# Kernel tuning notes

Measured on AMD Instinct MI355X. Metric: run time of the kernel, lower is better.

## Reference

```python
import jax, jax.numpy as jnp
import numpy as np

NUM_HEADS = 16
DIM_K = 128
DIM_V = 128
ROPE_BASE = 10000.0


def rope(x):
    # x: [..., seq, d]; rotate-half convention
    d = x.shape[-1]
    seq = x.shape[-2]
    half = d // 2
    inv_freq = 1.0 / (ROPE_BASE ** (jnp.arange(0, half, dtype=jnp.float32) / half))
    ang = jnp.arange(seq, dtype=jnp.float32)[:, None] * inv_freq[None, :]  # [seq, half]
    cos, sin = jnp.cos(ang), jnp.sin(ang)
    x1, x2 = x[..., :half], x[..., half:]
    return jnp.concatenate([x1 * cos - x2 * sin, x1 * sin + x2 * cos], axis=-1)


def setup_inputs() -> dict:
    key = jax.random.key(0)
    ks = jax.random.split(key, 8)
    B, S, D = 2, 2048, 2048
    s = lambda fan_in: 1.0 / np.sqrt(fan_in)
    return {
        'q_in': jax.random.normal(ks[0], (B, S, D), jnp.float32),
        'k_in': jax.random.normal(ks[1], (B, S, D), jnp.float32),
        'v_in': jax.random.normal(ks[2], (B, S, D), jnp.float32),
        'mask': jnp.zeros((B, S), dtype=bool),
        'Wq': jax.random.normal(ks[3], (D, NUM_HEADS * DIM_K), jnp.float32) * s(D),
        'bq': jnp.zeros((NUM_HEADS * DIM_K,), jnp.float32),
        'Wk': jax.random.normal(ks[4], (D, DIM_K), jnp.float32) * s(D),
        'bk': jnp.zeros((DIM_K,), jnp.float32),
        'Wv': jax.random.normal(ks[5], (D, DIM_V), jnp.float32) * s(D),
        'bv': jnp.zeros((DIM_V,), jnp.float32),
        'Wo': jax.random.normal(ks[6], (NUM_HEADS * DIM_V, D), jnp.float32) * s(NUM_HEADS * DIM_V),
        'bo': jnp.zeros((D,), jnp.float32),
    }


def reference(q_in, k_in, v_in, mask, Wq, bq, Wk, bk, Wv, bv, Wo, bo):
    B, Sq, _ = q_in.shape
    Sk = k_in.shape[1]
    # projections: multi-head Q, single shared K/V head (MQA)
    q = (q_in @ Wq + bq).reshape(B, Sq, NUM_HEADS, DIM_K).transpose(0, 2, 1, 3)  # [B,H,Sq,dk]
    k = k_in @ Wk + bk  # [B,Sk,dk]
    v = v_in @ Wv + bv  # [B,Sk,dv]
    # inline RoPE on q and k
    q = rope(q)
    k = rope(k)
    scores = jnp.einsum('bhqd,bkd->bhqk', q, k) / np.sqrt(DIM_K)  # [B,H,Sq,Sk]
    # padding mask: True means masked out
    scores = jnp.where(mask[:, None, None, :], -jnp.inf, scores)
    # causal mask
    causal = jnp.triu(jnp.ones((Sq, Sk), dtype=bool), k=1)
    scores = jnp.where(causal[None, None], -jnp.inf, scores)
    weights = jax.nn.softmax(scores, axis=-1)
    attn = jnp.einsum('bhqk,bkd->bhqd', weights, v)  # [B,H,Sq,dv]
    attn = attn.transpose(0, 2, 1, 3).reshape(B, Sq, NUM_HEADS * DIM_V)
    return attn @ Wo + bo
```

## Files before the change

kernel.cpp:

```cpp
#include <hip/hip_runtime.h>

#define NHEADS 16
#define DKV 128
#define BB 2
#define SS 2048
#define DD 2048

typedef __attribute__((ext_vector_type(8))) short bf16x8;
typedef __attribute__((ext_vector_type(4))) short bf16x4;
typedef __attribute__((ext_vector_type(4))) float f32x4;

#define QSCL 0.12752775f

__device__ __forceinline__ short f2bf(float x) {
  unsigned u = __builtin_bit_cast(unsigned, x);
  unsigned r = (u + 0x7fffu + ((u >> 16) & 1u)) >> 16;
  return (short)(unsigned short)r;
}
__device__ __forceinline__ float bf2f(short s) {
  unsigned u = ((unsigned)(unsigned short)s) << 16;
  return __builtin_bit_cast(float, u);
}
__device__ __forceinline__ unsigned pk2bf(float a, float b) {
#if __has_builtin(__builtin_amdgcn_cvt_pk_bf16_f32)
  typedef __attribute__((ext_vector_type(2))) __bf16 bf2_t;
  bf2_t r = __builtin_amdgcn_cvt_pk_bf16_f32(a, b);
  return __builtin_bit_cast(unsigned, r);
#else
  unsigned ua = __builtin_bit_cast(unsigned, a);
  unsigned ub = __builtin_bit_cast(unsigned, b);
  return ((ua + 0x8000u) >> 16) | ((ub + 0x8000u) & 0xffff0000u);
#endif
}
__device__ __forceinline__ float exp2fast(float x) {
#if __has_builtin(__builtin_amdgcn_exp2f)
  return __builtin_amdgcn_exp2f(x);
#else
  return exp2f(x);
#endif
}

__device__ __forceinline__ void async16(const void* g, void* l) {
  __builtin_amdgcn_global_load_lds(
      (__attribute__((address_space(1))) void*)g,
      (__attribute__((address_space(3))) void*)l, 16, 0, 0);
}

__global__ __launch_bounds__(256) void cvt_q(const float* __restrict__ x,
                                             short* __restrict__ y) {
  int idx = blockIdx.x * 256 + threadIdx.x;
  int g = idx * 8;
  float4 a = *(const float4*)(x + g);
  float4 b = *(const float4*)(x + g + 4);
  uint4 o = {pk2bf(a.x, a.y), pk2bf(a.z, a.w), pk2bf(b.x, b.y), pk2bf(b.z, b.w)};
  *(uint4*)(y + g) = o;
}

__global__ __launch_bounds__(256) void transpose_w(
    const float* __restrict__ W, short* __restrict__ Wt, int K, int N,
    float scale) {
  __shared__ float T[32][33];
  const int nt = blockIdx.x * 32;
  const int kt = blockIdx.y * 32;
  const int tx = threadIdx.x & 31;
  const int ty = threadIdx.x >> 5;
#pragma unroll
  for (int i = 0; i < 4; ++i)
    T[ty + i * 8][tx] = W[(size_t)(kt + ty + i * 8) * N + nt + tx];
  __syncthreads();
#pragma unroll
  for (int i = 0; i < 4; ++i)
    Wt[(size_t)(nt + ty + i * 8) * K + kt + tx] = f2bf(T[tx][ty + i * 8] * scale);
}

__global__ void mask_bias(const unsigned char* __restrict__ m,
                          float* __restrict__ mb) {
  int i = blockIdx.x * 256 + threadIdx.x;
  mb[i] = m[i] ? -1e30f : 0.0f;
}

template <int AMODE>
__global__ __launch_bounds__(256) void gemm_as(
    const void* __restrict__ Ap, const short* __restrict__ Bt,
    const float* __restrict__ bias, void* __restrict__ Cp,
    int M, int N, int K, int KC, int cmode, float bscale) {
  __shared__ __align__(16) short As[128 * 32];
  __shared__ __align__(16) short Bs[128 * 32];
  const int tid = threadIdx.x;
  const int bm = blockIdx.y * 128;
  const int bn = blockIdx.x * 128;
  const int kz = blockIdx.z;
  const int w = tid >> 6, lane = tid & 63;
  const int lm = lane & 15, q4 = lane >> 4;
  const int m0 = (w & 1) * 64, n0 = (w >> 1) * 64;

  f32x4 acc[4][4];
#pragma unroll
  for (int mi = 0; mi < 4; ++mi)
#pragma unroll
    for (int ni = 0; ni < 4; ++ni) acc[mi][ni] = (f32x4){0.f, 0.f, 0.f, 0.f};

  const int kbeg = kz * KC;
  const int kend = kbeg + KC;

  for (int k0 = kbeg; k0 < kend; k0 += 32) {
    __syncthreads();
    if (AMODE == 1) {
      const short* Ab = (const short*)Ap;
#pragma unroll
      for (int i = 0; i < 2; ++i) {
        int rA = (w * 2 + i) * 16 + (lane >> 2);
        int cA = (lane & 3) ^ (rA & 3);
        async16(Ab + (size_t)(bm + rA) * K + k0 + cA * 8, &As[(w * 2 + i) * 512]);
      }
    } else {
      const float* Af = (const float*)Ap;
      float4 av[4];
#pragma unroll
      for (int i = 0; i < 4; ++i) {
        int qd = tid + i * 256;
        int r = qd >> 3, cq = qd & 7;
        av[i] = *(const float4*)(Af + (size_t)(bm + r) * K + k0 + cq * 4);
      }
#pragma unroll
      for (int i = 0; i < 4; ++i) {
        int qd = tid + i * 256;
        int r = qd >> 3, cq = qd & 7;
        int ch = cq >> 1, hf = cq & 1;
        int pc = ch ^ (r & 3);
        bf16x4 t = {f2bf(av[i].x), f2bf(av[i].y), f2bf(av[i].z), f2bf(av[i].w)};
        *(bf16x4*)&As[r * 32 + pc * 8 + hf * 4] = t;
      }
    }
#pragma unroll
    for (int i = 0; i < 2; ++i) {
      int rB = (w * 2 + i) * 16 + (lane >> 2);
      int cB = (lane & 3) ^ (rB & 3);
      async16(Bt + (size_t)(bn + rB) * K + k0 + cB * 8, &Bs[(w * 2 + i) * 512]);
    }
    __syncthreads();

    bf16x8 af[4], bf[4];
#pragma unroll
    for (int mi = 0; mi < 4; ++mi)
      af[mi] = *(const bf16x8*)&As[(m0 + mi * 16 + lm) * 32 + ((q4 ^ (lm & 3)) * 8)];
#pragma unroll
    for (int ni = 0; ni < 4; ++ni)
      bf[ni] = *(const bf16x8*)&Bs[(n0 + ni * 16 + lm) * 32 + ((q4 ^ (lm & 3)) * 8)];
#pragma unroll
    for (int mi = 0; mi < 4; ++mi)
#pragma unroll
      for (int ni = 0; ni < 4; ++ni)
        acc[mi][ni] = __builtin_amdgcn_mfma_f32_16x16x32_bf16(
            af[mi], bf[ni], acc[mi][ni], 0, 0, 0);
  }

  if (cmode == 2) {
    float* Cf = (float*)Cp + (size_t)kz * M * N;
#pragma unroll
    for (int mi = 0; mi < 4; ++mi)
#pragma unroll
      for (int ni = 0; ni < 4; ++ni)
#pragma unroll
        for (int reg = 0; reg < 4; ++reg)
          Cf[(size_t)(bm + m0 + mi * 16 + q4 * 4 + reg) * N +
             (bn + n0 + ni * 16 + lm)] = acc[mi][ni][reg];
  } else {
#pragma unroll
    for (int mi = 0; mi < 4; ++mi)
#pragma unroll
      for (int ni = 0; ni < 4; ++ni)
#pragma unroll
        for (int reg = 0; reg < 4; ++reg) {
          int rowg = bm + m0 + mi * 16 + q4 * 4 + reg;
          int colg = bn + n0 + ni * 16 + lm;
          float val = acc[mi][ni][reg] + bias[colg] * bscale;
          if (cmode == 0)
            ((float*)Cp)[(size_t)rowg * N + colg] = val;
          else
            ((short*)Cp)[(size_t)rowg * N + colg] = f2bf(val);
        }
  }
}

#define SPLITK 4
__global__ __launch_bounds__(256) void kv_reduce(
    const float* __restrict__ kpart, const float* __restrict__ vpart,
    const float* __restrict__ bk, const float* __restrict__ bv,
    short* __restrict__ kp, short* __restrict__ vtb) {
  __shared__ float Kt[32][128];
  __shared__ short Vl[128][36];
  const int tid = threadIdx.x;
  const int r0 = blockIdx.x * 32;
#pragma unroll
  for (int i = 0; i < 16; ++i) {
    int e = tid + i * 256;
    int r = e >> 7, c = e & 127;
    float sk = 0.f, sv = 0.f;
#pragma unroll
    for (int z = 0; z < SPLITK; ++z) {
      sk += kpart[((size_t)z * 4096 + r0 + r) * 128 + c];
      sv += vpart[((size_t)z * 4096 + r0 + r) * 128 + c];
    }
    Kt[r][c] = sk + bk[c];
    Vl[c][r] = f2bf(sv + bv[c]);
  }
  __syncthreads();
#pragma unroll
  for (int i = 0; i < 8; ++i) {
    int e = tid + i * 256;
    int r = e >> 6, d = e & 63;
    float x1 = Kt[r][d], x2 = Kt[r][d + 64];
    float s = (float)((r0 + r) & (SS - 1));
    float ang = s * exp2fast((float)d * (-13.287712379549449f / 64.0f));
    float sn, cs;
    __sincosf(ang, &sn, &cs);
    kp[(size_t)(r0 + r) * 128 + d] = f2bf(x1 * cs - x2 * sn);
    kp[(size_t)(r0 + r) * 128 + d + 64] = f2bf(x1 * sn + x2 * cs);
  }
  const int b = r0 >> 11;
  const int j = tid >> 1, soff = (tid & 1) * 16;
  short* dst = vtb + ((size_t)b * 128 + j) * SS + (r0 & (SS - 1)) + soff;
#pragma unroll
  for (int t = 0; t < 2; ++t) {
    bf16x8 tmp;
#pragma unroll
    for (int u = 0; u < 8; ++u) tmp[u] = Vl[j][soff + t * 8 + u];
    *(bf16x8*)(dst + t * 8) = tmp;
  }
}

__global__ __launch_bounds__(256) void rope_q(short* __restrict__ qp) {
  int idx = blockIdx.x * 256 + threadIdx.x;
  int j8 = idx & 7;
  int h = (idx >> 3) & (NHEADS - 1);
  int s = (idx >> 7) & (SS - 1);
  int b = idx >> 18;
  short* base = qp + (((size_t)b * SS + s) * NHEADS + h) * DKV + j8 * 8;
  bf16x8 x1 = *(bf16x8*)base;
  bf16x8 x2 = *(bf16x8*)(base + 64);
  bf16x8 y1, y2;
#pragma unroll
  for (int j = 0; j < 8; ++j) {
    int d = j8 * 8 + j;
    float ang = (float)s * exp2fast((float)d * (-13.287712379549449f / 64.0f));
    float sn, cs;
    __sincosf(ang, &sn, &cs);
    float a = bf2f(x1[j]), bb2 = bf2f(x2[j]);
    y1[j] = f2bf(a * cs - bb2 * sn);
    y2[j] = f2bf(a * sn + bb2 * cs);
  }
  *(bf16x8*)base = y1;
  *(bf16x8*)(base + 64) = y2;
}

#define PSTR 40

__global__ __launch_bounds__(256, 2) void flash_kernel(
    const short* __restrict__ q, const short* __restrict__ k,
    const short* __restrict__ vt, const float* __restrict__ mb,
    short* __restrict__ out) {
  __shared__ __align__(16) short Kb[2][32 * 128];
  __shared__ __align__(16) short Vb[2][128 * 64];
  __shared__ __align__(16) short Ps[4][32 * PSTR];
  const int h = blockIdx.y, b = blockIdx.z;
  const int qx = b ? (int)blockIdx.x : 15 - (int)blockIdx.x;
  const int tid = threadIdx.x;
  const int w = tid >> 6, lane = tid & 63;
  const int lm = lane & 15, q4 = lane >> 4;
  const int qrow0 = qx * 128 + w * 32;

  bf16x8 qf[2][4];
#pragma unroll
  for (int ni = 0; ni < 2; ++ni)
#pragma unroll
    for (int ks = 0; ks < 4; ++ks)
      qf[ni][ks] = *(const bf16x8*)(q +
          ((size_t)b * SS + qrow0 + ni * 16 + lm) * (NHEADS * DKV) + h * DKV +
          ks * 32 + q4 * 8);

  bf16x8 onesb;
#pragma unroll
  for (int j = 0; j < 8; ++j) onesb[j] = (short)0x3F80;

  f32x4 O[8][2], Ol[2];
#pragma unroll
  for (int vi = 0; vi < 8; ++vi)
#pragma unroll
    for (int ni = 0; ni < 2; ++ni) O[vi][ni] = (f32x4){0.f, 0.f, 0.f, 0.f};
#pragma unroll
  for (int ni = 0; ni < 2; ++ni) Ol[ni] = (f32x4){0.f, 0.f, 0.f, 0.f};

  const int ktmax = 4 * qx + 4;
  const size_t kbase = (size_t)b * SS;

  {
#pragma unroll
    for (int i = 0; i < 2; ++i) {
      int r = (w * 2 + i) * 4 + (lane >> 4);
      int c = (lane & 15) ^ (r & 7);
      async16(k + (kbase + r) * DKV + c * 8, &Kb[0][(w * 2 + i) * 512]);
    }
#pragma unroll
    for (int i = 0; i < 4; ++i) {
      int rV = (w * 4 + i) * 8 + (lane >> 3);
      int cV = (lane & 7) ^ (rV & 7);
      async16(vt + ((size_t)b * DKV + rV) * SS + cV * 8, &Vb[0][(w * 4 + i) * 512]);
    }
  }
  f32x4 mc0 = *(const f32x4*)(mb + kbase + q4 * 4);
  f32x4 mc1 = *(const f32x4*)(mb + kbase + 16 + q4 * 4);

  for (int kt = 0; kt < ktmax; ++kt) {
    __syncthreads();

    f32x4 mn0, mn1;
    if (kt + 1 < ktmax) {
      const int t = kt + 1;
#pragma unroll
      for (int i = 0; i < 2; ++i) {
        int r = (w * 2 + i) * 4 + (lane >> 4);
        int c = (lane & 15) ^ (r & 7);
        async16(k + (kbase + (size_t)t * 32 + r) * DKV + c * 8,
                &Kb[t & 1][(w * 2 + i) * 512]);
      }
      if (kt & 1) {
#pragma unroll
        for (int i = 0; i < 4; ++i) {
          int rV = (w * 4 + i) * 8 + (lane >> 3);
          int cV = (lane & 7) ^ (rV & 7);
          async16(vt + ((size_t)b * DKV + rV) * SS + (size_t)t * 32 + cV * 8,
                  &Vb[(t >> 1) & 1][(w * 4 + i) * 512]);
        }
      }
      mn0 = *(const f32x4*)(mb + kbase + (size_t)t * 32 + q4 * 4);
      mn1 = *(const f32x4*)(mb + kbase + (size_t)t * 32 + 16 + q4 * 4);
    }

    const short* Kc = Kb[kt & 1];
    f32x4 sacc[2][2];
#pragma unroll
    for (int mi = 0; mi < 2; ++mi)
#pragma unroll
      for (int ni = 0; ni < 2; ++ni) sacc[mi][ni] = (f32x4){0.f, 0.f, 0.f, 0.f};
#pragma unroll
    for (int mi = 0; mi < 2; ++mi)
#pragma unroll
      for (int ks = 0; ks < 4; ++ks) {
        bf16x8 kf = *(const bf16x8*)&Kc[(mi * 16 + lm) * 128 +
                                        (((ks * 4 + q4) ^ (lm & 7)) << 3)];
#pragma unroll
        for (int ni = 0; ni < 2; ++ni)
          sacc[mi][ni] = __builtin_amdgcn_mfma_f32_16x16x32_bf16(
              kf, qf[ni][ks], sacc[mi][ni], 0, 0, 0);
      }

    const bool diag = (kt >= 4 * qx);
#pragma unroll
    for (int mi = 0; mi < 2; ++mi) {
      f32x4 mbv = mi ? mc1 : mc0;
#pragma unroll
      for (int ni = 0; ni < 2; ++ni) {
        float pv[4];
#pragma unroll
        for (int reg = 0; reg < 4; ++reg) {
          float s = sacc[mi][ni][reg] + mbv[reg];
          if (diag) {
            int kg = kt * 32 + mi * 16 + q4 * 4 + reg;
            int qg = qrow0 + ni * 16 + lm;
            if (kg > qg) s = -1e30f;
          }
          pv[reg] = exp2fast(s);
        }
        uint2 pkd = {pk2bf(pv[0], pv[1]), pk2bf(pv[2], pv[3])};
        *(uint2*)&Ps[w][(ni * 16 + lm) * PSTR + mi * 16 + q4 * 4] = pkd;
      }
    }
    mc0 = mn0;
    mc1 = mn1;

    const short* Vc = Vb[(kt >> 1) & 1];
    const int hf4 = (kt & 1) * 4;
    bf16x8 pf[2];
#pragma unroll
    for (int ni = 0; ni < 2; ++ni) {
      pf[ni] = *(const bf16x8*)&Ps[w][(ni * 16 + lm) * PSTR + q4 * 8];
      Ol[ni] = __builtin_amdgcn_mfma_f32_16x16x32_bf16(pf[ni], onesb, Ol[ni], 0, 0, 0);
    }
#pragma unroll
    for (int vi = 0; vi < 8; ++vi) {
      bf16x8 vf = *(const bf16x8*)&Vc[(vi * 16 + lm) * 64 +
                                      (((hf4 + q4) ^ (lm & 7)) << 3)];
#pragma unroll
      for (int ni = 0; ni < 2; ++ni)
        O[vi][ni] = __builtin_amdgcn_mfma_f32_16x16x32_bf16(
            pf[ni], vf, O[vi][ni], 0, 0, 0);
    }
  }

  __syncthreads();
  float* Wr = (float*)&Vb[0][0] + w * 2048;
  float linv[2][4];
#pragma unroll
  for (int ni = 0; ni < 2; ++ni)
#pragma unroll
    for (int reg = 0; reg < 4; ++reg) linv[ni][reg] = 1.0f / Ol[ni][reg];

#pragma unroll
  for (int qd = 0; qd < 4; ++qd) {
#pragma unroll
    for (int v2 = 0; v2 < 2; ++v2) {
      int vi = qd * 2 + v2;
#pragma unroll
      for (int ni = 0; ni < 2; ++ni)
#pragma unroll
        for (int reg = 0; reg < 4; ++reg)
          Wr[(ni * 16 + q4 * 4 + reg) * 34 + v2 * 16 + lm] =
              O[vi][ni][reg] * linv[ni][reg];
    }
    int r = lane & 31, hh = lane >> 5;
    f32x4 t0 = *(const f32x4*)&Wr[r * 34 + hh * 16];
    f32x4 t1 = *(const f32x4*)&Wr[r * 34 + hh * 16 + 4];
    f32x4 t2 = *(const f32x4*)&Wr[r * 34 + hh * 16 + 8];
    f32x4 t3 = *(const f32x4*)&Wr[r * 34 + hh * 16 + 12];
    size_t oaddr = ((size_t)b * SS + qx * 128 + w * 32 + r) * (NHEADS * DKV) +
                   h * DKV + qd * 32 + hh * 16;
    uint4 o0 = {pk2bf(t0[0], t0[1]), pk2bf(t0[2], t0[3]),
                pk2bf(t1[0], t1[1]), pk2bf(t1[2], t1[3])};
    uint4 o1 = {pk2bf(t2[0], t2[1]), pk2bf(t2[2], t2[3]),
                pk2bf(t3[0], t3[1]), pk2bf(t3[2], t3[3])};
    *(uint4*)(out + oaddr) = o0;
    *(uint4*)(out + oaddr + 8) = o1;
  }
}

extern "C" void kernel_launch(void* const* d_in, const int* in_sizes, int n_in,
                              void* d_out, int out_size, void* d_ws, size_t ws_size,
                              hipStream_t stream) {
  const float* q_in = (const float*)d_in[0];
  const float* k_in = (const float*)d_in[1];
  const float* v_in = (const float*)d_in[2];
  const unsigned char* mask = (const unsigned char*)d_in[3];
  const float* Wq = (const float*)d_in[4];
  const float* bq = (const float*)d_in[5];
  const float* Wk = (const float*)d_in[6];
  const float* bk = (const float*)d_in[7];
  const float* Wv = (const float*)d_in[8];
  const float* bv = (const float*)d_in[9];
  const float* Wo = (const float*)d_in[10];
  const float* bo = (const float*)d_in[11];

  const int M = BB * SS;
  short* Wqt = (short*)d_ws;
  short* Wot = Wqt + (size_t)DD * DD;
  short* Wkt = Wot + (size_t)DD * DD;
  short* Wvt = Wkt + (size_t)DKV * DD;
  short* qb  = Wvt + (size_t)DKV * DD;
  short* qp  = qb + (size_t)M * DD;
  short* kp  = qp + (size_t)M * DD;
  short* vtb = kp + (size_t)M * DKV;
  float* mb  = (float*)(vtb + (size_t)BB * DKV * SS);
  float* kpart = mb + (size_t)BB * SS;
  float* vpart = kpart + (size_t)SPLITK * M * DKV;
  short* ap = qb;

  cvt_q<<<M * DD / (8 * 256), 256, 0, stream>>>(q_in, qb);
  transpose_w<<<dim3(DD / 32, DD / 32), 256, 0, stream>>>(Wq, Wqt, DD, DD, QSCL);
  transpose_w<<<dim3(DKV / 32, DD / 32), 256, 0, stream>>>(Wk, Wkt, DD, DKV, 1.0f);
  transpose_w<<<dim3(DKV / 32, DD / 32), 256, 0, stream>>>(Wv, Wvt, DD, DKV, 1.0f);
  transpose_w<<<dim3(DD / 32, DD / 32), 256, 0, stream>>>(Wo, Wot, DD, DD, 1.0f);
  mask_bias<<<BB * SS / 256, 256, 0, stream>>>(mask, mb);

  gemm_as<1><<<dim3(DD / 128, M / 128, 1), 256, 0, stream>>>(
      qb, Wqt, bq, qp, M, DD, DD, DD, 1, QSCL);
  gemm_as<0><<<dim3(1, M / 128, SPLITK), 256, 0, stream>>>(
      k_in, Wkt, nullptr, kpart, M, DKV, DD, DD / SPLITK, 2, 1.0f);
  gemm_as<0><<<dim3(1, M / 128, SPLITK), 256, 0, stream>>>(
      v_in, Wvt, nullptr, vpart, M, DKV, DD, DD / SPLITK, 2, 1.0f);
  kv_reduce<<<M / 32, 256, 0, stream>>>(kpart, vpart, bk, bv, kp, vtb);
  rope_q<<<(BB * SS * NHEADS * 8) / 256, 256, 0, stream>>>(qp);

  flash_kernel<<<dim3(16, NHEADS, BB), 256, 0, stream>>>(qp, kp, vtb, mb, ap);

  gemm_as<1><<<dim3(DD / 128, M / 128, 1), 256, 0, stream>>>(
      ap, Wot, bo, d_out, M, DD, DD, DD, 0, 1.0f);
}
```

Measured before the change: 429.8 us.

## Split long causal query tiles across two KV halves and merge partials

The flash kernel is relaunched as a 1D grid of 768 blocks. Query tiles 8-15 are split into two KV ranges, so no block runs more than 32 key tiles, and blocks are ordered so heavy work is issued first. Partial outputs are written in fp16 together with row sums, and a new combine kernel merges the two halves. This evens out causal load imbalance, at the cost of an extra launch, extra global traffic for the partials, and fp16 rounding of the intermediate values. The merge adds the normalized halves weighted only by their row sums, which assumes both halves share a consistent softmax max (e.g. a fixed offset rather than a running max).

```diff
diff --git a/kernel.cpp b/kernel.cpp
--- a/kernel.cpp
+++ b/kernel.cpp
@@ -9,6 +9,7 @@
 typedef __attribute__((ext_vector_type(8))) short bf16x8;
 typedef __attribute__((ext_vector_type(4))) short bf16x4;
 typedef __attribute__((ext_vector_type(4))) float f32x4;
+typedef __attribute__((ext_vector_type(8))) _Float16 f16x8;
 
 #define QSCL 0.12752775f
 
@@ -30,6 +31,18 @@
   unsigned ua = __builtin_bit_cast(unsigned, a);
   unsigned ub = __builtin_bit_cast(unsigned, b);
   return ((ua + 0x8000u) >> 16) | ((ub + 0x8000u) & 0xffff0000u);
+#endif
+}
+__device__ __forceinline__ unsigned pkf16(float a, float b) {
+#if __has_builtin(__builtin_amdgcn_cvt_pkrtz)
+  typedef __attribute__((ext_vector_type(2))) __fp16 h2_t;
+  h2_t r = __builtin_amdgcn_cvt_pkrtz(a, b);
+  return __builtin_bit_cast(unsigned, r);
+#else
+  _Float16 ha = (_Float16)a, hb = (_Float16)b;
+  unsigned short ua = __builtin_bit_cast(unsigned short, ha);
+  unsigned short ub = __builtin_bit_cast(unsigned short, hb);
+  return (unsigned)ua | ((unsigned)ub << 16);
 #endif
 }
 __device__ __forceinline__ float exp2fast(float x) {
@@ -259,12 +272,25 @@
 __global__ __launch_bounds__(256, 2) void flash_kernel(
     const short* __restrict__ q, const short* __restrict__ k,
     const short* __restrict__ vt, const float* __restrict__ mb,
-    short* __restrict__ out) {
+    short* __restrict__ out, short* __restrict__ pO, float* __restrict__ pL) {
   __shared__ __align__(16) short Kb[2][32 * 128];
   __shared__ __align__(16) short Vb[2][128 * 64];
   __shared__ __align__(16) short Ps[4][32 * PSTR];
-  const int h = blockIdx.y, b = blockIdx.z;
-  const int qx = b ? (int)blockIdx.x : 15 - (int)blockIdx.x;
+  const int j = blockIdx.x;
+  const int cls = j >> 5, hb = j & 31;
+  int qx, c;
+  if (cls < 8) {
+    qx = cls + 8; c = 0;
+  } else {
+    int kk = (cls - 8) >> 1;
+    if ((cls & 1) == 0) { qx = 15 - kk; c = 1; }
+    else                { qx = 7 - kk;  c = 0; }
+  }
+  const int h = hb & 15, b = hb >> 4;
+  const int kt0 = c ? 32 : 0;
+  int kend = 4 * qx + 4;
+  if (c == 0 && kend > 32) kend = 32;
+
   const int tid = threadIdx.x;
   const int w = tid >> 6, lane = tid & 63;
   const int lm = lane & 15, q4 = lane >> 4;
@@ -281,7 +307,7 @@
 
   bf16x8 onesb;
 #pragma unroll
-  for (int j = 0; j < 8; ++j) onesb[j] = (short)0x3F80;
+  for (int jj = 0; jj < 8; ++jj) onesb[jj] = (short)0x3F80;
 
   f32x4 O[8][2], Ol[2];
 #pragma unroll
@@ -291,37 +317,38 @@
 #pragma unroll
   for (int ni = 0; ni < 2; ++ni) Ol[ni] = (f32x4){0.f, 0.f, 0.f, 0.f};
 
-  const int ktmax = 4 * qx + 4;
   const size_t kbase = (size_t)b * SS;
 
   {
 #pragma unroll
     for (int i = 0; i < 2; ++i) {
       int r = (w * 2 + i) * 4 + (lane >> 4);
-      int c = (lane & 15) ^ (r & 7);
-      async16(k + (kbase + r) * DKV + c * 8, &Kb[0][(w * 2 + i) * 512]);
+      int cc = (lane & 15) ^ (r & 7);
+      async16(k + (kbase + (size_t)kt0 * 32 + r) * DKV + cc * 8,
+              &Kb[0][(w * 2 + i) * 512]);
     }
 #pragma unroll
     for (int i = 0; i < 4; ++i) {
       int rV = (w * 4 + i) * 8 + (lane >> 3);
       int cV = (lane & 7) ^ (rV & 7);
-      async16(vt + ((size_t)b * DKV + rV) * SS + cV * 8, &Vb[0][(w * 4 + i) * 512]);
-    }
-  }
-  f32x4 mc0 = *(const f32x4*)(mb + kbase + q4 * 4);
-  f32x4 mc1 = *(const f32x4*)(mb + kbase + 16 + q4 * 4);
-
-  for (int kt = 0; kt < ktmax; ++kt) {
+      async16(vt + ((size_t)b * DKV + rV) * SS + (size_t)kt0 * 32 + cV * 8,
+              &Vb[0][(w * 4 + i) * 512]);
+    }
+  }
+  f32x4 mc0 = *(const f32x4*)(mb + kbase + (size_t)kt0 * 32 + q4 * 4);
+  f32x4 mc1 = *(const f32x4*)(mb + kbase + (size_t)kt0 * 32 + 16 + q4 * 4);
+
+  for (int kt = kt0; kt < kend; ++kt) {
     __syncthreads();
 
     f32x4 mn0, mn1;
-    if (kt + 1 < ktmax) {
+    if (kt + 1 < kend) {
       const int t = kt + 1;
 #pragma unroll
       for (int i = 0; i < 2; ++i) {
         int r = (w * 2 + i) * 4 + (lane >> 4);
-        int c = (lane & 15) ^ (r & 7);
-        async16(k + (kbase + (size_t)t * 32 + r) * DKV + c * 8,
+        int cc = (lane & 15) ^ (r & 7);
+        async16(k + (kbase + (size_t)t * 32 + r) * DKV + cc * 8,
                 &Kb[t & 1][(w * 2 + i) * 512]);
       }
       if (kt & 1) {
@@ -406,6 +433,26 @@
 #pragma unroll
     for (int reg = 0; reg < 4; ++reg) linv[ni][reg] = 1.0f / Ol[ni][reg];
 
+  const bool split = (qx >= 8);
+  short* obase;
+  int ostr;
+  if (split) {
+    int slot = ((b * 16 + h) * 8 + (qx - 8)) * 2 + c;
+    obase = pO + (size_t)slot * (128 * 128);
+    ostr = 128;
+    if (lm == 0) {
+      float* dl = pL + (size_t)slot * 128 + w * 32;
+#pragma unroll
+      for (int ni = 0; ni < 2; ++ni)
+#pragma unroll
+        for (int reg = 0; reg < 4; ++reg)
+          dl[ni * 16 + q4 * 4 + reg] = Ol[ni][reg];
+    }
+  } else {
+    obase = out + ((size_t)b * SS + qx * 128) * (NHEADS * DKV) + h * DKV;
+    ostr = NHEADS * DKV;
+  }
+
 #pragma unroll
   for (int qd = 0; qd < 4; ++qd) {
 #pragma unroll
@@ -423,14 +470,53 @@
     f32x4 t1 = *(const f32x4*)&Wr[r * 34 + hh * 16 + 4];
     f32x4 t2 = *(const f32x4*)&Wr[r * 34 + hh * 16 + 8];
     f32x4 t3 = *(const f32x4*)&Wr[r * 34 + hh * 16 + 12];
-    size_t oaddr = ((size_t)b * SS + qx * 128 + w * 32 + r) * (NHEADS * DKV) +
-                   h * DKV + qd * 32 + hh * 16;
-    uint4 o0 = {pk2bf(t0[0], t0[1]), pk2bf(t0[2], t0[3]),
-                pk2bf(t1[0], t1[1]), pk2bf(t1[2], t1[3])};
-    uint4 o1 = {pk2bf(t2[0], t2[1]), pk2bf(t2[2], t2[3]),
-                pk2bf(t3[0], t3[1]), pk2bf(t3[2], t3[3])};
-    *(uint4*)(out + oaddr) = o0;
-    *(uint4*)(out + oaddr + 8) = o1;
+    size_t oaddr = (size_t)(w * 32 + r) * ostr + qd * 32 + hh * 16;
+    uint4 o0, o1;
+    if (split) {
+      o0 = (uint4){pkf16(t0[0], t0[1]), pkf16(t0[2], t0[3]),
+                   pkf16(t1[0], t1[1]), pkf16(t1[2], t1[3])};
+      o1 = (uint4){pkf16(t2[0], t2[1]), pkf16(t2[2], t2[3]),
+                   pkf16(t3[0], t3[1]), pkf16(t3[2], t3[3])};
+    } else {
+      o0 = (uint4){pk2bf(t0[0], t0[1]), pk2bf(t0[2], t0[3]),
+                   pk2bf(t1[0], t1[1]), pk2bf(t1[2], t1[3])};
+      o1 = (uint4){pk2bf(t2[0], t2[1]), pk2bf(t2[2], t2[3]),
+                   pk2bf(t3[0], t3[1]), pk2bf(t3[2], t3[3])};
+    }
+    *(uint4*)(obase + oaddr) = o0;
+    *(uint4*)(obase + oaddr + 8) = o1;
+  }
+}
+
+__global__ __launch_bounds__(256) void combine(
+    const short* __restrict__ pO, const float* __restrict__ pL,
+    short* __restrict__ out) {
+  const int qxi = blockIdx.x, h = blockIdx.y, b = blockIdx.z;
+  const int qx = 8 + qxi;
+  const int slot2 = ((b * 16 + h) * 8 + qxi) * 2;
+  const _Float16* p0 = (const _Float16*)(pO + (size_t)slot2 * (128 * 128));
+  const _Float16* p1 = p0 + 128 * 128;
+  const float* l0 = pL + (size_t)slot2 * 128;
+  const float* l1 = l0 + 128;
+  const int t = threadIdx.x;
+  const int row = t >> 1, half = t & 1;
+  const float w0 = l0[row], w1 = l1[row];
+  const float inv = 1.0f / (w0 + w1);
+  const float a0 = w0 * inv, a1 = w1 * inv;
+  const int off = row * 128 + half * 64;
+  short* dst = out + ((size_t)(b * SS + qx * 128 + row)) * (NHEADS * DKV) +
+               h * DKV + half * 64;
+#pragma unroll
+  for (int v = 0; v < 8; ++v) {
+    f16x8 x0 = *(const f16x8*)(p0 + off + v * 8);
+    f16x8 x1 = *(const f16x8*)(p1 + off + v * 8);
+    float r[8];
+#pragma unroll
+    for (int u = 0; u < 8; ++u)
+      r[u] = (float)x0[u] * a0 + (float)x1[u] * a1;
+    uint4 o = {pk2bf(r[0], r[1]), pk2bf(r[2], r[3]),
+               pk2bf(r[4], r[5]), pk2bf(r[6], r[7])};
+    *(uint4*)(dst + v * 8) = o;
   }
 }
 
@@ -462,7 +548,9 @@
   float* mb  = (float*)(vtb + (size_t)BB * DKV * SS);
   float* kpart = mb + (size_t)BB * SS;
   float* vpart = kpart + (size_t)SPLITK * M * DKV;
+  float* pL = vpart + (size_t)SPLITK * M * DKV;
   short* ap = qb;
+  short* pO = (short*)kpart;
 
   cvt_q<<<M * DD / (8 * 256), 256, 0, stream>>>(q_in, qb);
   transpose_w<<<dim3(DD / 32, DD / 32), 256, 0, stream>>>(Wq, Wqt, DD, DD, QSCL);
@@ -480,7 +568,8 @@
   kv_reduce<<<M / 32, 256, 0, stream>>>(kpart, vpart, bk, bv, kp, vtb);
   rope_q<<<(BB * SS * NHEADS * 8) / 256, 256, 0, stream>>>(qp);
 
-  flash_kernel<<<dim3(16, NHEADS, BB), 256, 0, stream>>>(qp, kp, vtb, mb, ap);
+  flash_kernel<<<dim3(768), 256, 0, stream>>>(qp, kp, vtb, mb, ap, pO, pL);
+  combine<<<dim3(8, NHEADS, BB), 256, 0, stream>>>(pO, pL, ap);
 
   gemm_as<1><<<dim3(DD / 128, M / 128, 1), 256, 0, stream>>>(
       ap, Wot, bo, d_out, M, DD, DD, DD, 0, 1.0f);
```

After: 419.4 us. -2.4%, faster.
